# Optimization experiments

Hardware: AMD Instinct MI355X
Metric: run time of the kernel (lower is better)

## Reference

```python
import jax, jax.numpy as jnp
import numpy as np

TOPK = 16  # module init arg
EPS = 1e-12  # F.normalize eps


def setup_inputs() -> dict:
    key = jax.random.key(0)
    k1, k2, k3 = jax.random.split(key, 3)
    b, c, h, w = 2, 256, 96, 96
    rc = max(c // 4, 16)  # reduced_channels = 64
    x = jax.random.normal(k1, (b, c, h, w), dtype=jnp.float32)
    # 1x1 convs are channel-mixing matmuls; store weights as [out_ch, in_ch]
    w_reduce = jax.random.normal(k2, (rc, c), dtype=jnp.float32) * 0.05
    w_proj = jax.random.normal(k3, (c, rc), dtype=jnp.float32) * 0.05
    return {"x": x, "w_reduce": w_reduce, "w_proj": w_proj}


def reference(x, w_reduce, w_proj):
    b, c, h, w = x.shape
    n = h * w
    # reduce: 1x1 conv == channel matmul -> [b, rc, N]
    feat = jnp.einsum('rc,bchw->brhw', w_reduce, x).reshape(b, -1, n)
    # F.normalize(dim=1): divide by max(L2-norm over channels, eps)
    nrm = jnp.maximum(jnp.sqrt(jnp.sum(feat * feat, axis=1, keepdims=True)), EPS)
    nf = jnp.transpose(feat / nrm, (0, 2, 1))  # [b, N, rc]
    # cosine similarity matrix [b, N, N]
    sim = jnp.einsum('bnr,bmr->bnm', nf, nf)
    k = min(TOPK, n)
    _, idx = jax.lax.top_k(sim, k)  # [b, N, k]
    # gather top-k neighbor features and average -> [b, N, rc]
    corr = jax.vmap(lambda f, i: f[i].mean(axis=1))(nf, idx)
    # proj: 1x1 conv back to C channels, NCHW layout
    enhanced = jnp.einsum('cr,bnr->bnc', w_proj, corr)
    enhanced = jnp.transpose(enhanced, (0, 2, 1)).reshape(b, c, h, w)
    return x + enhanced
```

## Files before the change

kernel.cpp:

```cpp
#include <hip/hip_runtime.h>
#include <cstdint>
#include <cstddef>

#define NPIX 9216
#define NB 2
#define NC 256
#define RC 64
#define TK 16
#define NROWS (NB * NPIX)
#define CT 128
#define ECOLS 1152
#define NTE 9
#define MAXC 128
#define MARGIN 0.008f

typedef unsigned short ushort_t;
typedef unsigned int uint_t;
typedef __bf16 bf16x8 __attribute__((ext_vector_type(8)));
typedef float f32x4 __attribute__((ext_vector_type(4)));

__device__ __forceinline__ uint_t f2bf(float x) {
  uint_t u = __float_as_uint(x);
  return (u + 0x7FFFu + ((u >> 16) & 1u)) >> 16;
}

__device__ __forceinline__ uint_t ordu(float v) {
  uint_t u = __float_as_uint(v);
  return (u & 0x80000000u) ? ~u : (u | 0x80000000u);
}

__global__ __launch_bounds__(256) void k_reduce(
    const float* __restrict__ x, const float* __restrict__ wr,
    float* __restrict__ feat4) {
  __shared__ float wl[64 * 16];
  const int bi = blockIdx.x;
  const int pg = bi >> 4, rq = (bi >> 2) & 3, cq = bi & 3;
  const int tid = threadIdx.x;
  {
    const int cl = tid >> 2, rg = (tid & 3) * 4;
#pragma unroll
    for (int i = 0; i < 4; ++i)
      wl[cl * 16 + rg + i] = wr[(size_t)(rq * 16 + rg + i) * NC + cq * 64 + cl];
  }
  __syncthreads();

  const int p = pg * 256 + tid;
  const int b = p >= NPIX;
  const int n = p - b * NPIX;
  const float* xp = x + (size_t)b * NC * NPIX + (size_t)cq * 64 * NPIX + n;

  float4 acc[4];
#pragma unroll
  for (int i = 0; i < 4; ++i) acc[i] = make_float4(0.f, 0.f, 0.f, 0.f);

  for (int c = 0; c < 64; ++c) {
    const float xv = xp[(size_t)c * NPIX];
    const float4* w4 = (const float4*)(wl + c * 16);
#pragma unroll
    for (int i = 0; i < 4; ++i) {
      float4 w = w4[i];
      acc[i].x += w.x * xv; acc[i].y += w.y * xv;
      acc[i].z += w.z * xv; acc[i].w += w.w * xv;
    }
  }
  float4* o = (float4*)(feat4 + (((size_t)(rq * 4 + cq)) * NROWS + p) * 16);
#pragma unroll
  for (int i = 0; i < 4; ++i) o[i] = acc[i];
}

__global__ __launch_bounds__(256) void k_normsplit(
    const float* __restrict__ feat4, float* __restrict__ nf,
    ushort_t* __restrict__ hi) {
  const int t = blockIdx.x * 256 + threadIdx.x;
  const int p = t >> 2, q = t & 3;
  float4 v[4];
#pragma unroll
  for (int i = 0; i < 4; ++i) v[i] = make_float4(0.f, 0.f, 0.f, 0.f);
#pragma unroll
  for (int pt = 0; pt < 4; ++pt) {
    const float4* fp = (const float4*)(feat4 + (((size_t)(q * 4 + pt)) * NROWS + p) * 16);
#pragma unroll
    for (int i = 0; i < 4; ++i) {
      float4 a = fp[i];
      v[i].x += a.x; v[i].y += a.y; v[i].z += a.z; v[i].w += a.w;
    }
  }
  float ssq = 0.f;
#pragma unroll
  for (int i = 0; i < 4; ++i)
    ssq += v[i].x * v[i].x + v[i].y * v[i].y + v[i].z * v[i].z + v[i].w * v[i].w;
  ssq += __shfl_xor(ssq, 1);
  ssq += __shfl_xor(ssq, 2);
  const float inv = 1.f / fmaxf(sqrtf(ssq), 1e-12f);

  float s[16];
#pragma unroll
  for (int i = 0; i < 4; ++i) {
    s[i * 4 + 0] = v[i].x * inv; s[i * 4 + 1] = v[i].y * inv;
    s[i * 4 + 2] = v[i].z * inv; s[i * 4 + 3] = v[i].w * inv;
  }
  float4* no = (float4*)(nf + (size_t)p * RC + q * 16);
#pragma unroll
  for (int i = 0; i < 4; ++i)
    no[i] = make_float4(s[i * 4], s[i * 4 + 1], s[i * 4 + 2], s[i * 4 + 3]);

  uint_t hs[16];
#pragma unroll
  for (int i = 0; i < 16; ++i) hs[i] = f2bf(s[i]);
  uint4* ho = (uint4*)(hi + (size_t)p * RC + q * 16);
#pragma unroll
  for (int h = 0; h < 2; ++h)
    ho[h] = make_uint4(hs[h*8+0] | (hs[h*8+1] << 16), hs[h*8+2] | (hs[h*8+3] << 16),
                       hs[h*8+4] | (hs[h*8+5] << 16), hs[h*8+6] | (hs[h*8+7] << 16));
}

__global__ __launch_bounds__(256) void k_sim_max(
    const ushort_t* __restrict__ nf_hi, float* __restrict__ tmax) {
  __shared__ ushort_t sh[CT * 72];
  const int rb = blockIdx.x >> 3, q = blockIdx.x & 7;
  const int tid = threadIdx.x, wave = tid >> 6, lane = tid & 63;
  const int n = lane & 15, quad = lane >> 4;
  const int r0 = rb * 128 + wave * 32 + n, r1 = r0 + 16;
  const int b = rb >= 72;
  const size_t cbase = (size_t)b * NPIX;

  const bf16x8 bh00 = *(const bf16x8*)(nf_hi + (size_t)r0 * 64 + quad * 8);
  const bf16x8 bh01 = *(const bf16x8*)(nf_hi + (size_t)r0 * 64 + 32 + quad * 8);
  const bf16x8 bh10 = *(const bf16x8*)(nf_hi + (size_t)r1 * 64 + quad * 8);
  const bf16x8 bh11 = *(const bf16x8*)(nf_hi + (size_t)r1 * 64 + 32 + quad * 8);

  const int sc = tid >> 1, sseg = (tid & 1) * 32;
  float cm0 = -1e30f, cm1 = -1e30f;

  for (int t = 0; t < NTE; ++t) {
    const int cb = q * ECOLS + t * CT;
    __syncthreads();
    {
      const uint4* g = (const uint4*)(nf_hi + (cbase + cb + sc) * 64 + sseg);
      uint4* d = (uint4*)(sh + sc * 72 + sseg);
#pragma unroll
      for (int i = 0; i < 4; ++i) d[i] = g[i];
    }
    __syncthreads();

#pragma unroll 2
    for (int st = 0; st < 8; ++st) {
      const ushort_t* ap = sh + (st * 16 + n) * 72 + quad * 8;
      bf16x8 ah0 = *(const bf16x8*)ap;
      bf16x8 ah1 = *(const bf16x8*)(ap + 32);
      f32x4 z = {0.f, 0.f, 0.f, 0.f};
      f32x4 a0 = __builtin_amdgcn_mfma_f32_16x16x32_bf16(ah0, bh00, z, 0, 0, 0);
      a0 = __builtin_amdgcn_mfma_f32_16x16x32_bf16(ah1, bh01, a0, 0, 0, 0);
      f32x4 a1 = __builtin_amdgcn_mfma_f32_16x16x32_bf16(ah0, bh10, z, 0, 0, 0);
      a1 = __builtin_amdgcn_mfma_f32_16x16x32_bf16(ah1, bh11, a1, 0, 0, 0);
      cm0 = fmaxf(cm0, fmaxf(fmaxf(a0[0], a0[1]), fmaxf(a0[2], a0[3])));
      cm1 = fmaxf(cm1, fmaxf(fmaxf(a1[0], a1[1]), fmaxf(a1[2], a1[3])));
    }
    if (t % 3 == 2) {
      const int cn = t / 3;
      tmax[(size_t)r0 * 96 + (q * 4 + quad) * 3 + cn] = cm0;
      tmax[(size_t)r1 * 96 + (q * 4 + quad) * 3 + cn] = cm1;
      cm0 = -1e30f; cm1 = -1e30f;
    }
  }
}

__global__ __launch_bounds__(256) void k_thresh(
    const float* __restrict__ tmax, float* __restrict__ Tb) {
  const int wave = threadIdx.x >> 6, lane = threadIdx.x & 63;
  const int row = blockIdx.x * 4 + wave;
  const float* tp = tmax + (size_t)row * 96;
  float v0 = tp[lane];
  float v1 = (lane < 32) ? tp[64 + lane] : -1e30f;
  float m = -1e30f;
#pragma unroll
  for (int k = 0; k < TK; ++k) {
    float c = fmaxf(v0, v1);
#pragma unroll
    for (int d = 1; d < 64; d <<= 1) c = fmaxf(c, __shfl_xor(c, d));
    m = c;
    if (v0 == m) v0 = -1e30f;
    if (v1 == m) v1 = -1e30f;
  }
  if (lane == 0) Tb[row] = m - MARGIN;
}

__global__ __launch_bounds__(256) void k_collect(
    const ushort_t* __restrict__ nf_hi, const float* __restrict__ Tb,
    int* __restrict__ cidx, int* __restrict__ rowcnt) {
  __shared__ ushort_t sh[CT * 72];
  const int rb = blockIdx.x >> 3, q = blockIdx.x & 7;
  const int tid = threadIdx.x, wave = tid >> 6, lane = tid & 63;
  const int n = lane & 15, quad = lane >> 4;
  const int r0 = rb * 128 + wave * 32 + n, r1 = r0 + 16;
  const int b = rb >= 72;
  const size_t cbase = (size_t)b * NPIX;

  const bf16x8 bh00 = *(const bf16x8*)(nf_hi + (size_t)r0 * 64 + quad * 8);
  const bf16x8 bh01 = *(const bf16x8*)(nf_hi + (size_t)r0 * 64 + 32 + quad * 8);
  const bf16x8 bh10 = *(const bf16x8*)(nf_hi + (size_t)r1 * 64 + quad * 8);
  const bf16x8 bh11 = *(const bf16x8*)(nf_hi + (size_t)r1 * 64 + 32 + quad * 8);

  const float T0 = Tb[r0], T1 = Tb[r1];
  const int sc = tid >> 1, sseg = (tid & 1) * 32;

  for (int t = 0; t < NTE; ++t) {
    const int cb = q * ECOLS + t * CT;
    __syncthreads();
    {
      const uint4* g = (const uint4*)(nf_hi + (cbase + cb + sc) * 64 + sseg);
      uint4* d = (uint4*)(sh + sc * 72 + sseg);
#pragma unroll
      for (int i = 0; i < 4; ++i) d[i] = g[i];
    }
    __syncthreads();

#pragma unroll 2
    for (int st = 0; st < 8; ++st) {
      const ushort_t* ap = sh + (st * 16 + n) * 72 + quad * 8;
      bf16x8 ah0 = *(const bf16x8*)ap;
      bf16x8 ah1 = *(const bf16x8*)(ap + 32);
      f32x4 z = {0.f, 0.f, 0.f, 0.f};
      f32x4 a0 = __builtin_amdgcn_mfma_f32_16x16x32_bf16(ah0, bh00, z, 0, 0, 0);
      a0 = __builtin_amdgcn_mfma_f32_16x16x32_bf16(ah1, bh01, a0, 0, 0, 0);
      f32x4 a1 = __builtin_amdgcn_mfma_f32_16x16x32_bf16(ah0, bh10, z, 0, 0, 0);
      a1 = __builtin_amdgcn_mfma_f32_16x16x32_bf16(ah1, bh11, a1, 0, 0, 0);

      const int c0 = cb + st * 16 + quad * 4;
      const float mx0 = fmaxf(fmaxf(a0[0], a0[1]), fmaxf(a0[2], a0[3]));
      if (mx0 >= T0) {
#pragma unroll
        for (int r = 0; r < 4; ++r)
          if (a0[r] >= T0) {
            const int slot = atomicAdd(rowcnt + r0, 1);
            if (slot < MAXC) cidx[(size_t)r0 * MAXC + slot] = c0 + r;
          }
      }
      const float mx1 = fmaxf(fmaxf(a1[0], a1[1]), fmaxf(a1[2], a1[3]));
      if (mx1 >= T1) {
#pragma unroll
        for (int r = 0; r < 4; ++r)
          if (a1[r] >= T1) {
            const int slot = atomicAdd(rowcnt + r1, 1);
            if (slot < MAXC) cidx[(size_t)r1 * MAXC + slot] = c0 + r;
          }
      }
    }
  }
}

__global__ __launch_bounds__(256) void k_merge_gather(
    const float* __restrict__ nf, const int* __restrict__ cidx,
    const int* __restrict__ rowcnt, float* __restrict__ corr) {
  const int wave = threadIdx.x >> 6, lane = threadIdx.x & 63;
  const int row0 = blockIdx.x * 16 + wave * 4;
#pragma unroll 1
  for (int rr = 0; rr < 4; ++rr) {
    const int row = row0 + rr;
    const int b = row >= NPIX;
    const int rl = row - b * NPIX;
    const float* nfb = nf + (size_t)b * NPIX * RC;
    const int C = min(rowcnt[row], MAXC);

    float4 rv[16];
    const float4* r4 = (const float4*)(nf + (size_t)row * RC);
#pragma unroll
    for (int i = 0; i < 16; ++i) rv[i] = r4[i];

    const int* cp = cidx + (size_t)row * MAXC;
    unsigned long long k0 = 0, k1 = 0;
    {
      const int c0 = (lane < C) ? cp[lane] : rl;
      const float4* g = (const float4*)(nfb + (size_t)c0 * RC);
      float s = 0.f;
#pragma unroll
      for (int i = 0; i < 16; ++i) {
        float4 a = g[i];
        s += a.x * rv[i].x + a.y * rv[i].y + a.z * rv[i].z + a.w * rv[i].w;
      }
      if (lane < C)
        k0 = ((unsigned long long)ordu(s) << 32) | (uint_t)(~(uint_t)c0);
    }
    if (C > 64) {
      const int c1 = (64 + lane < C) ? cp[64 + lane] : rl;
      const float4* g = (const float4*)(nfb + (size_t)c1 * RC);
      float s = 0.f;
#pragma unroll
      for (int i = 0; i < 16; ++i) {
        float4 a = g[i];
        s += a.x * rv[i].x + a.y * rv[i].y + a.z * rv[i].z + a.w * rv[i].w;
      }
      if (64 + lane < C)
        k1 = ((unsigned long long)ordu(s) << 32) | (uint_t)(~(uint_t)c1);
    }

    int sel[TK];
#pragma unroll
    for (int t = 0; t < TK; ++t) {
      unsigned long long m = k0 > k1 ? k0 : k1;
#pragma unroll
      for (int d = 1; d < 64; d <<= 1) {
        unsigned long long o = __shfl_xor(m, d);
        m = (o > m) ? o : m;
      }
      sel[t] = (m == 0) ? rl : (int)(~(uint_t)(m & 0xFFFFFFFFull));
      if (k0 == m) k0 = 0;
      else if (k1 == m) k1 = 0;
    }

    float acc = 0.f;
#pragma unroll
    for (int t = 0; t < TK; ++t)
      acc += nfb[(size_t)sel[t] * RC + lane];
    corr[(size_t)row * RC + lane] = acc * 0.0625f;
  }
}

__global__ __launch_bounds__(256) void k_proj_add(
    const float* __restrict__ x, const float* __restrict__ wp,
    const float* __restrict__ corr, float* __restrict__ out) {
  const int pg = blockIdx.x >> 3, cq = blockIdx.x & 7;
  const int tid = threadIdx.x;

  __shared__ float wl[32 * RC];
  {
    const float4* src = (const float4*)(wp + (size_t)cq * 32 * RC);
    float4* dst = (float4*)wl;
#pragma unroll
    for (int i = 0; i < 2; ++i) dst[i * 256 + tid] = src[i * 256 + tid];
  }

  const int p = pg * 256 + tid;
  const int b = p >= NPIX;
  const int n = p - b * NPIX;

  float4 cr[16];
  const float4* c4 = (const float4*)(corr + (size_t)p * RC);
#pragma unroll
  for (int i = 0; i < 16; ++i) cr[i] = c4[i];
  __syncthreads();

  const size_t xb = (size_t)b * NC * NPIX + n;
  for (int cl = 0; cl < 32; ++cl) {
    const float4* w4 = (const float4*)(wl + cl * RC);
    float s = 0.f;
#pragma unroll
    for (int i = 0; i < 16; ++i) {
      float4 w = w4[i];
      s += w.x * cr[i].x + w.y * cr[i].y + w.z * cr[i].z + w.w * cr[i].w;
    }
    const int c = cq * 32 + cl;
    const size_t oi = xb + (size_t)c * NPIX;
    out[oi] = x[oi] + s;
  }
}

extern "C" void kernel_launch(void* const* d_in, const int* in_sizes, int n_in,
                              void* d_out, int out_size, void* d_ws, size_t ws_size,
                              hipStream_t stream) {
  const float* x = (const float*)d_in[0];
  const float* wr = (const float*)d_in[1];
  const float* wp = (const float*)d_in[2];
  float* out = (float*)d_out;

  char* ws = (char*)d_ws;
  float* feat4 = (float*)ws;
  float* tmax = (float*)ws;
  float* corr = (float*)ws;
  float* nf = (float*)(ws + 18874368);
  ushort_t* nf_hi = (ushort_t*)(ws + 23592960);
  float* Tb = (float*)(ws + 25952256);
  int* rowcnt = (int*)(ws + 26025984);
  int* cidx = (int*)(ws + 26099712);

  hipLaunchKernelGGL(k_reduce, dim3(1152), dim3(256), 0, stream, x, wr, feat4);
  hipLaunchKernelGGL(k_normsplit, dim3(288), dim3(256), 0, stream, feat4, nf, nf_hi);
  hipLaunchKernelGGL(k_sim_max, dim3(1152), dim3(256), 0, stream, nf_hi, tmax);
  hipLaunchKernelGGL(k_thresh, dim3(NROWS / 4), dim3(256), 0, stream, tmax, Tb);
  hipMemsetAsync(rowcnt, 0, NROWS * sizeof(int), stream);
  hipLaunchKernelGGL(k_collect, dim3(1152), dim3(256), 0, stream,
                     nf_hi, Tb, cidx, rowcnt);
  hipLaunchKernelGGL(k_merge_gather, dim3(1152), dim3(256), 0, stream,
                     nf, cidx, rowcnt, corr);
  hipLaunchKernelGGL(k_proj_add, dim3(576), dim3(256), 0, stream, x, wp, corr, out);
}
```

Baseline: 314.9 us.

## Restructure sim tiles: waves split columns, all rows in registers, swizzled LDS

In the similarity-max and collect kernels, each wave now holds B fragments for all 128 rows of the block and covers two 16-column strips of the staged tile. Before, each wave held 32 rows and swept all 128 columns. Shared memory drops its 72-element padding in favour of an XOR swizzle to avoid bank conflicts. Collect now issues one atomic per 4-value group using popcount instead of one per hit. Merge-gather maps one row per wave across more blocks. The chunk-max layout grows from 96 to 128 chunks per row, which changes the threshold input, and the larger register footprint may lower occupancy.

```diff
diff --git a/kernel.cpp b/kernel.cpp
--- a/kernel.cpp
+++ b/kernel.cpp
@@ -9,8 +9,10 @@
 #define TK 16
 #define NROWS (NB * NPIX)
 #define CT 128
+#define NQ 8
 #define ECOLS 1152
 #define NTE 9
+#define NCHUNK 128
 #define MAXC 128
 #define MARGIN 0.008f
 
@@ -114,64 +116,77 @@
                        hs[h*8+4] | (hs[h*8+5] << 16), hs[h*8+6] | (hs[h*8+7] << 16));
 }
 
+__device__ __forceinline__ void stage_tile(
+    const ushort_t* __restrict__ nf_hi, size_t cbase, int cb,
+    ushort_t* sh, int tid) {
+  const int srow = tid >> 1, shalf = tid & 1;
+  const uint4* g4 = (const uint4*)(nf_hi + (cbase + (size_t)(cb + srow)) * 64 + shalf * 32);
+  uint4 v0 = g4[0], v1 = g4[1], v2 = g4[2], v3 = g4[3];
+  ushort_t* rowp = sh + srow * 64;
+  const int rx = srow & 7;
+  *(uint4*)(rowp + (((shalf * 4 + 0) ^ rx) * 8)) = v0;
+  *(uint4*)(rowp + (((shalf * 4 + 1) ^ rx) * 8)) = v1;
+  *(uint4*)(rowp + (((shalf * 4 + 2) ^ rx) * 8)) = v2;
+  *(uint4*)(rowp + (((shalf * 4 + 3) ^ rx) * 8)) = v3;
+}
+
 __global__ __launch_bounds__(256) void k_sim_max(
     const ushort_t* __restrict__ nf_hi, float* __restrict__ tmax) {
-  __shared__ ushort_t sh[CT * 72];
+  __shared__ ushort_t sh[CT * 64];
   const int rb = blockIdx.x >> 3, q = blockIdx.x & 7;
   const int tid = threadIdx.x, wave = tid >> 6, lane = tid & 63;
   const int n = lane & 15, quad = lane >> 4;
-  const int r0 = rb * 128 + wave * 32 + n, r1 = r0 + 16;
+  const int rowbase = rb * 128 + n;
   const int b = rb >= 72;
   const size_t cbase = (size_t)b * NPIX;
 
-  const bf16x8 bh00 = *(const bf16x8*)(nf_hi + (size_t)r0 * 64 + quad * 8);
-  const bf16x8 bh01 = *(const bf16x8*)(nf_hi + (size_t)r0 * 64 + 32 + quad * 8);
-  const bf16x8 bh10 = *(const bf16x8*)(nf_hi + (size_t)r1 * 64 + quad * 8);
-  const bf16x8 bh11 = *(const bf16x8*)(nf_hi + (size_t)r1 * 64 + 32 + quad * 8);
-
-  const int sc = tid >> 1, sseg = (tid & 1) * 32;
-  float cm0 = -1e30f, cm1 = -1e30f;
+  bf16x8 bh0[8], bh1[8];
+#pragma unroll
+  for (int g = 0; g < 8; ++g) {
+    const ushort_t* rp = nf_hi + (size_t)(rowbase + g * 16) * 64;
+    bh0[g] = *(const bf16x8*)(rp + quad * 8);
+    bh1[g] = *(const bf16x8*)(rp + 32 + quad * 8);
+  }
+
+  const int x0 = (quad ^ (n & 7)) * 8;
+  const int x1 = ((quad + 4) ^ (n & 7)) * 8;
+
+  float cm[8];
+#pragma unroll
+  for (int g = 0; g < 8; ++g) cm[g] = -1e30f;
 
   for (int t = 0; t < NTE; ++t) {
-    const int cb = q * ECOLS + t * CT;
     __syncthreads();
-    {
-      const uint4* g = (const uint4*)(nf_hi + (cbase + cb + sc) * 64 + sseg);
-      uint4* d = (uint4*)(sh + sc * 72 + sseg);
-#pragma unroll
-      for (int i = 0; i < 4; ++i) d[i] = g[i];
-    }
+    stage_tile(nf_hi, cbase, q * ECOLS + t * CT, sh, tid);
     __syncthreads();
 
-#pragma unroll 2
-    for (int st = 0; st < 8; ++st) {
-      const ushort_t* ap = sh + (st * 16 + n) * 72 + quad * 8;
-      bf16x8 ah0 = *(const bf16x8*)ap;
-      bf16x8 ah1 = *(const bf16x8*)(ap + 32);
-      f32x4 z = {0.f, 0.f, 0.f, 0.f};
-      f32x4 a0 = __builtin_amdgcn_mfma_f32_16x16x32_bf16(ah0, bh00, z, 0, 0, 0);
-      a0 = __builtin_amdgcn_mfma_f32_16x16x32_bf16(ah1, bh01, a0, 0, 0, 0);
-      f32x4 a1 = __builtin_amdgcn_mfma_f32_16x16x32_bf16(ah0, bh10, z, 0, 0, 0);
-      a1 = __builtin_amdgcn_mfma_f32_16x16x32_bf16(ah1, bh11, a1, 0, 0, 0);
-      cm0 = fmaxf(cm0, fmaxf(fmaxf(a0[0], a0[1]), fmaxf(a0[2], a0[3])));
-      cm1 = fmaxf(cm1, fmaxf(fmaxf(a1[0], a1[1]), fmaxf(a1[2], a1[3])));
-    }
-    if (t % 3 == 2) {
-      const int cn = t / 3;
-      tmax[(size_t)r0 * 96 + (q * 4 + quad) * 3 + cn] = cm0;
-      tmax[(size_t)r1 * 96 + (q * 4 + quad) * 3 + cn] = cm1;
-      cm0 = -1e30f; cm1 = -1e30f;
-    }
-  }
+#pragma unroll
+    for (int p = 0; p < 2; ++p) {
+      const int st = wave * 2 + p;
+      const ushort_t* ap = sh + (st * 16 + n) * 64;
+      const bf16x8 ah0 = *(const bf16x8*)(ap + x0);
+      const bf16x8 ah1 = *(const bf16x8*)(ap + x1);
+#pragma unroll
+      for (int g = 0; g < 8; ++g) {
+        f32x4 z = {0.f, 0.f, 0.f, 0.f};
+        f32x4 a = __builtin_amdgcn_mfma_f32_16x16x32_bf16(ah0, bh0[g], z, 0, 0, 0);
+        a = __builtin_amdgcn_mfma_f32_16x16x32_bf16(ah1, bh1[g], a, 0, 0, 0);
+        cm[g] = fmaxf(fmaxf(a[0], a[1]), fmaxf(fmaxf(a[2], a[3]), cm[g]));
+      }
+    }
+  }
+#pragma unroll
+  for (int g = 0; g < 8; ++g)
+    tmax[(size_t)(rowbase + g * 16) * NCHUNK + q * 16 + wave * 4 + quad] = cm[g];
 }
 
 __global__ __launch_bounds__(256) void k_thresh(
     const float* __restrict__ tmax, float* __restrict__ Tb) {
   const int wave = threadIdx.x >> 6, lane = threadIdx.x & 63;
   const int row = blockIdx.x * 4 + wave;
-  const float* tp = tmax + (size_t)row * 96;
+  const float* tp = tmax + (size_t)row * NCHUNK;
   float v0 = tp[lane];
-  float v1 = (lane < 32) ? tp[64 + lane] : -1e30f;
+  float v1 = tp[64 + lane];
   float m = -1e30f;
 #pragma unroll
   for (int k = 0; k < TK; ++k) {
@@ -188,62 +203,58 @@
 __global__ __launch_bounds__(256) void k_collect(
     const ushort_t* __restrict__ nf_hi, const float* __restrict__ Tb,
     int* __restrict__ cidx, int* __restrict__ rowcnt) {
-  __shared__ ushort_t sh[CT * 72];
+  __shared__ ushort_t sh[CT * 64];
   const int rb = blockIdx.x >> 3, q = blockIdx.x & 7;
   const int tid = threadIdx.x, wave = tid >> 6, lane = tid & 63;
   const int n = lane & 15, quad = lane >> 4;
-  const int r0 = rb * 128 + wave * 32 + n, r1 = r0 + 16;
+  const int rowbase = rb * 128 + n;
   const int b = rb >= 72;
   const size_t cbase = (size_t)b * NPIX;
 
-  const bf16x8 bh00 = *(const bf16x8*)(nf_hi + (size_t)r0 * 64 + quad * 8);
-  const bf16x8 bh01 = *(const bf16x8*)(nf_hi + (size_t)r0 * 64 + 32 + quad * 8);
-  const bf16x8 bh10 = *(const bf16x8*)(nf_hi + (size_t)r1 * 64 + quad * 8);
-  const bf16x8 bh11 = *(const bf16x8*)(nf_hi + (size_t)r1 * 64 + 32 + quad * 8);
-
-  const float T0 = Tb[r0], T1 = Tb[r1];
-  const int sc = tid >> 1, sseg = (tid & 1) * 32;
+  bf16x8 bh0[8], bh1[8];
+  float T[8];
+#pragma unroll
+  for (int g = 0; g < 8; ++g) {
+    const ushort_t* rp = nf_hi + (size_t)(rowbase + g * 16) * 64;
+    bh0[g] = *(const bf16x8*)(rp + quad * 8);
+    bh1[g] = *(const bf16x8*)(rp + 32 + quad * 8);
+    T[g] = Tb[rowbase + g * 16];
+  }
+
+  const int x0 = (quad ^ (n & 7)) * 8;
+  const int x1 = ((quad + 4) ^ (n & 7)) * 8;
 
   for (int t = 0; t < NTE; ++t) {
     const int cb = q * ECOLS + t * CT;
     __syncthreads();
-    {
-      const uint4* g = (const uint4*)(nf_hi + (cbase + cb + sc) * 64 + sseg);
-      uint4* d = (uint4*)(sh + sc * 72 + sseg);
-#pragma unroll
-      for (int i = 0; i < 4; ++i) d[i] = g[i];
-    }
+    stage_tile(nf_hi, cbase, cb, sh, tid);
     __syncthreads();
 
-#pragma unroll 2
-    for (int st = 0; st < 8; ++st) {
-      const ushort_t* ap = sh + (st * 16 + n) * 72 + quad * 8;
-      bf16x8 ah0 = *(const bf16x8*)ap;
-      bf16x8 ah1 = *(const bf16x8*)(ap + 32);
-      f32x4 z = {0.f, 0.f, 0.f, 0.f};
-      f32x4 a0 = __builtin_amdgcn_mfma_f32_16x16x32_bf16(ah0, bh00, z, 0, 0, 0);
-      a0 = __builtin_amdgcn_mfma_f32_16x16x32_bf16(ah1, bh01, a0, 0, 0, 0);
-      f32x4 a1 = __builtin_amdgcn_mfma_f32_16x16x32_bf16(ah0, bh10, z, 0, 0, 0);
-      a1 = __builtin_amdgcn_mfma_f32_16x16x32_bf16(ah1, bh11, a1, 0, 0, 0);
-
+#pragma unroll
+    for (int p = 0; p < 2; ++p) {
+      const int st = wave * 2 + p;
+      const ushort_t* ap = sh + (st * 16 + n) * 64;
+      const bf16x8 ah0 = *(const bf16x8*)(ap + x0);
+      const bf16x8 ah1 = *(const bf16x8*)(ap + x1);
       const int c0 = cb + st * 16 + quad * 4;
-      const float mx0 = fmaxf(fmaxf(a0[0], a0[1]), fmaxf(a0[2], a0[3]));
-      if (mx0 >= T0) {
-#pragma unroll
-        for (int r = 0; r < 4; ++r)
-          if (a0[r] >= T0) {
-            const int slot = atomicAdd(rowcnt + r0, 1);
-            if (slot < MAXC) cidx[(size_t)r0 * MAXC + slot] = c0 + r;
-          }
-      }
-      const float mx1 = fmaxf(fmaxf(a1[0], a1[1]), fmaxf(a1[2], a1[3]));
-      if (mx1 >= T1) {
-#pragma unroll
-        for (int r = 0; r < 4; ++r)
-          if (a1[r] >= T1) {
-            const int slot = atomicAdd(rowcnt + r1, 1);
-            if (slot < MAXC) cidx[(size_t)r1 * MAXC + slot] = c0 + r;
-          }
+#pragma unroll
+      for (int g = 0; g < 8; ++g) {
+        f32x4 z = {0.f, 0.f, 0.f, 0.f};
+        f32x4 a = __builtin_amdgcn_mfma_f32_16x16x32_bf16(ah0, bh0[g], z, 0, 0, 0);
+        a = __builtin_amdgcn_mfma_f32_16x16x32_bf16(ah1, bh1[g], a, 0, 0, 0);
+        const float Tg = T[g];
+        const int m = (a[0] >= Tg) | ((a[1] >= Tg) << 1) |
+                      ((a[2] >= Tg) << 2) | ((a[3] >= Tg) << 3);
+        if (m) {
+          const int rg = rowbase + g * 16;
+          int slot = atomicAdd(rowcnt + rg, __popc(m));
+#pragma unroll
+          for (int r = 0; r < 4; ++r)
+            if (m & (1 << r)) {
+              if (slot < MAXC) cidx[(size_t)rg * MAXC + slot] = c0 + r;
+              ++slot;
+            }
+        }
       }
     }
   }
@@ -253,67 +264,63 @@
     const float* __restrict__ nf, const int* __restrict__ cidx,
     const int* __restrict__ rowcnt, float* __restrict__ corr) {
   const int wave = threadIdx.x >> 6, lane = threadIdx.x & 63;
-  const int row0 = blockIdx.x * 16 + wave * 4;
-#pragma unroll 1
-  for (int rr = 0; rr < 4; ++rr) {
-    const int row = row0 + rr;
-    const int b = row >= NPIX;
-    const int rl = row - b * NPIX;
-    const float* nfb = nf + (size_t)b * NPIX * RC;
-    const int C = min(rowcnt[row], MAXC);
-
-    float4 rv[16];
-    const float4* r4 = (const float4*)(nf + (size_t)row * RC);
-#pragma unroll
-    for (int i = 0; i < 16; ++i) rv[i] = r4[i];
-
-    const int* cp = cidx + (size_t)row * MAXC;
-    unsigned long long k0 = 0, k1 = 0;
-    {
-      const int c0 = (lane < C) ? cp[lane] : rl;
-      const float4* g = (const float4*)(nfb + (size_t)c0 * RC);
-      float s = 0.f;
-#pragma unroll
-      for (int i = 0; i < 16; ++i) {
-        float4 a = g[i];
-        s += a.x * rv[i].x + a.y * rv[i].y + a.z * rv[i].z + a.w * rv[i].w;
-      }
-      if (lane < C)
-        k0 = ((unsigned long long)ordu(s) << 32) | (uint_t)(~(uint_t)c0);
-    }
-    if (C > 64) {
-      const int c1 = (64 + lane < C) ? cp[64 + lane] : rl;
-      const float4* g = (const float4*)(nfb + (size_t)c1 * RC);
-      float s = 0.f;
-#pragma unroll
-      for (int i = 0; i < 16; ++i) {
-        float4 a = g[i];
-        s += a.x * rv[i].x + a.y * rv[i].y + a.z * rv[i].z + a.w * rv[i].w;
-      }
-      if (64 + lane < C)
-        k1 = ((unsigned long long)ordu(s) << 32) | (uint_t)(~(uint_t)c1);
-    }
-
-    int sel[TK];
-#pragma unroll
-    for (int t = 0; t < TK; ++t) {
-      unsigned long long m = k0 > k1 ? k0 : k1;
-#pragma unroll
-      for (int d = 1; d < 64; d <<= 1) {
-        unsigned long long o = __shfl_xor(m, d);
-        m = (o > m) ? o : m;
-      }
-      sel[t] = (m == 0) ? rl : (int)(~(uint_t)(m & 0xFFFFFFFFull));
-      if (k0 == m) k0 = 0;
-      else if (k1 == m) k1 = 0;
-    }
-
-    float acc = 0.f;
-#pragma unroll
-    for (int t = 0; t < TK; ++t)
-      acc += nfb[(size_t)sel[t] * RC + lane];
-    corr[(size_t)row * RC + lane] = acc * 0.0625f;
-  }
+  const int row = blockIdx.x * 4 + wave;
+  const int b = row >= NPIX;
+  const int rl = row - b * NPIX;
+  const float* nfb = nf + (size_t)b * NPIX * RC;
+  const int C = min(rowcnt[row], MAXC);
+
+  float4 rv[16];
+  const float4* r4 = (const float4*)(nf + (size_t)row * RC);
+#pragma unroll
+  for (int i = 0; i < 16; ++i) rv[i] = r4[i];
+
+  const int* cp = cidx + (size_t)row * MAXC;
+  unsigned long long k0 = 0, k1 = 0;
+  {
+    const int c0 = (lane < C) ? cp[lane] : rl;
+    const float4* g = (const float4*)(nfb + (size_t)c0 * RC);
+    float s = 0.f;
+#pragma unroll
+    for (int i = 0; i < 16; ++i) {
+      float4 a = g[i];
+      s += a.x * rv[i].x + a.y * rv[i].y + a.z * rv[i].z + a.w * rv[i].w;
+    }
+    if (lane < C)
+      k0 = ((unsigned long long)ordu(s) << 32) | (uint_t)(~(uint_t)c0);
+  }
+  if (C > 64) {
+    const int c1 = (64 + lane < C) ? cp[64 + lane] : rl;
+    const float4* g = (const float4*)(nfb + (size_t)c1 * RC);
+    float s = 0.f;
+#pragma unroll
+    for (int i = 0; i < 16; ++i) {
+      float4 a = g[i];
+      s += a.x * rv[i].x + a.y * rv[i].y + a.z * rv[i].z + a.w * rv[i].w;
+    }
+    if (64 + lane < C)
+      k1 = ((unsigned long long)ordu(s) << 32) | (uint_t)(~(uint_t)c1);
+  }
+
+  int sel[TK];
+#pragma unroll
+  for (int t = 0; t < TK; ++t) {
+    unsigned long long m = k0 > k1 ? k0 : k1;
+#pragma unroll
+    for (int d = 1; d < 64; d <<= 1) {
+      unsigned long long o = __shfl_xor(m, d);
+      m = (o > m) ? o : m;
+    }
+    sel[t] = (m == 0) ? rl : (int)(~(uint_t)(m & 0xFFFFFFFFull));
+    if (k0 == m) k0 = 0;
+    else if (k1 == m) k1 = 0;
+  }
+
+  float acc = 0.f;
+#pragma unroll
+  for (int t = 0; t < TK; ++t)
+    acc += nfb[(size_t)sel[t] * RC + lane];
+  corr[(size_t)row * RC + lane] = acc * 0.0625f;
 }
 
 __global__ __launch_bounds__(256) void k_proj_add(
@@ -380,7 +387,7 @@
   hipMemsetAsync(rowcnt, 0, NROWS * sizeof(int), stream);
   hipLaunchKernelGGL(k_collect, dim3(1152), dim3(256), 0, stream,
                      nf_hi, Tb, cidx, rowcnt);
-  hipLaunchKernelGGL(k_merge_gather, dim3(1152), dim3(256), 0, stream,
+  hipLaunchKernelGGL(k_merge_gather, dim3(NROWS / 4), dim3(256), 0, stream,
                      nf, cidx, rowcnt, corr);
   hipLaunchKernelGGL(k_proj_add, dim3(576), dim3(256), 0, stream, x, wp, corr, out);
 }
```

Result: slower. 366.3 us (+16.3%).

## Buffer candidates in LDS and replace iterative top-k with radix-select ballot

Applied to the files above, without the earlier changes.

k_collect now appends candidate columns to per-row shared-memory lists using one LDS atomic per group of hits. Each row block then flushes its lists to global memory with a single global atomic per row, replacing one global atomic per hit. k_merge_gather assigns one row per wave and selects the 16 largest keys with a 64-bit bitwise radix search built on ballots, instead of 16 rounds of shuffle-based max reduction. This adds LDS use and a 64-step ballot loop. Ties at the threshold could produce a different ordering of selected indices, but the mean over the selected rows does not depend on order.

```diff
diff --git a/kernel.cpp b/kernel.cpp
--- a/kernel.cpp
+++ b/kernel.cpp
@@ -12,6 +12,7 @@
 #define ECOLS 1152
 #define NTE 9
 #define MAXC 128
+#define LCAP 128
 #define MARGIN 0.008f
 
 typedef unsigned short ushort_t;
@@ -189,12 +190,17 @@
     const ushort_t* __restrict__ nf_hi, const float* __restrict__ Tb,
     int* __restrict__ cidx, int* __restrict__ rowcnt) {
   __shared__ ushort_t sh[CT * 72];
+  __shared__ ushort_t lst[128][LCAP + 1];
+  __shared__ int lcnt[128];
   const int rb = blockIdx.x >> 3, q = blockIdx.x & 7;
   const int tid = threadIdx.x, wave = tid >> 6, lane = tid & 63;
   const int n = lane & 15, quad = lane >> 4;
-  const int r0 = rb * 128 + wave * 32 + n, r1 = r0 + 16;
+  const int rl0 = wave * 32 + n, rl1 = rl0 + 16;
+  const int r0 = rb * 128 + rl0, r1 = r0 + 16;
   const int b = rb >= 72;
   const size_t cbase = (size_t)b * NPIX;
+
+  if (tid < 128) lcnt[tid] = 0;
 
   const bf16x8 bh00 = *(const bf16x8*)(nf_hi + (size_t)r0 * 64 + quad * 8);
   const bf16x8 bh01 = *(const bf16x8*)(nf_hi + (size_t)r0 * 64 + 32 + quad * 8);
@@ -227,24 +233,38 @@
       a1 = __builtin_amdgcn_mfma_f32_16x16x32_bf16(ah1, bh11, a1, 0, 0, 0);
 
       const int c0 = cb + st * 16 + quad * 4;
-      const float mx0 = fmaxf(fmaxf(a0[0], a0[1]), fmaxf(a0[2], a0[3]));
-      if (mx0 >= T0) {
+      const int m0 = (a0[0] >= T0) | ((a0[1] >= T0) << 1) |
+                     ((a0[2] >= T0) << 2) | ((a0[3] >= T0) << 3);
+      if (m0) {
+        int slot = atomicAdd(&lcnt[rl0], __popc(m0));
 #pragma unroll
         for (int r = 0; r < 4; ++r)
-          if (a0[r] >= T0) {
-            const int slot = atomicAdd(rowcnt + r0, 1);
-            if (slot < MAXC) cidx[(size_t)r0 * MAXC + slot] = c0 + r;
+          if (m0 & (1 << r)) {
+            if (slot < LCAP) lst[rl0][slot] = (ushort_t)(c0 + r);
+            ++slot;
           }
       }
-      const float mx1 = fmaxf(fmaxf(a1[0], a1[1]), fmaxf(a1[2], a1[3]));
-      if (mx1 >= T1) {
+      const int m1 = (a1[0] >= T1) | ((a1[1] >= T1) << 1) |
+                     ((a1[2] >= T1) << 2) | ((a1[3] >= T1) << 3);
+      if (m1) {
+        int slot = atomicAdd(&lcnt[rl1], __popc(m1));
 #pragma unroll
         for (int r = 0; r < 4; ++r)
-          if (a1[r] >= T1) {
-            const int slot = atomicAdd(rowcnt + r1, 1);
-            if (slot < MAXC) cidx[(size_t)r1 * MAXC + slot] = c0 + r;
+          if (m1 & (1 << r)) {
+            if (slot < LCAP) lst[rl1][slot] = (ushort_t)(c0 + r);
+            ++slot;
           }
       }
+    }
+  }
+  __syncthreads();
+  if (tid < 128) {
+    const int row = rb * 128 + tid;
+    const int cnt = min(lcnt[tid], LCAP);
+    int base = atomicAdd(rowcnt + row, cnt);
+    for (int j = 0; j < cnt; ++j) {
+      const int gs = base + j;
+      if (gs < MAXC) cidx[(size_t)row * MAXC + gs] = (int)lst[tid][j];
     }
   }
 }
@@ -252,68 +272,78 @@
 __global__ __launch_bounds__(256) void k_merge_gather(
     const float* __restrict__ nf, const int* __restrict__ cidx,
     const int* __restrict__ rowcnt, float* __restrict__ corr) {
+  __shared__ ushort_t selc[4][TK];
   const int wave = threadIdx.x >> 6, lane = threadIdx.x & 63;
-  const int row0 = blockIdx.x * 16 + wave * 4;
-#pragma unroll 1
-  for (int rr = 0; rr < 4; ++rr) {
-    const int row = row0 + rr;
-    const int b = row >= NPIX;
-    const int rl = row - b * NPIX;
-    const float* nfb = nf + (size_t)b * NPIX * RC;
-    const int C = min(rowcnt[row], MAXC);
-
-    float4 rv[16];
-    const float4* r4 = (const float4*)(nf + (size_t)row * RC);
-#pragma unroll
-    for (int i = 0; i < 16; ++i) rv[i] = r4[i];
-
-    const int* cp = cidx + (size_t)row * MAXC;
-    unsigned long long k0 = 0, k1 = 0;
-    {
-      const int c0 = (lane < C) ? cp[lane] : rl;
-      const float4* g = (const float4*)(nfb + (size_t)c0 * RC);
-      float s = 0.f;
-#pragma unroll
-      for (int i = 0; i < 16; ++i) {
-        float4 a = g[i];
-        s += a.x * rv[i].x + a.y * rv[i].y + a.z * rv[i].z + a.w * rv[i].w;
-      }
-      if (lane < C)
-        k0 = ((unsigned long long)ordu(s) << 32) | (uint_t)(~(uint_t)c0);
-    }
-    if (C > 64) {
-      const int c1 = (64 + lane < C) ? cp[64 + lane] : rl;
-      const float4* g = (const float4*)(nfb + (size_t)c1 * RC);
-      float s = 0.f;
-#pragma unroll
-      for (int i = 0; i < 16; ++i) {
-        float4 a = g[i];
-        s += a.x * rv[i].x + a.y * rv[i].y + a.z * rv[i].z + a.w * rv[i].w;
-      }
-      if (64 + lane < C)
-        k1 = ((unsigned long long)ordu(s) << 32) | (uint_t)(~(uint_t)c1);
-    }
-
-    int sel[TK];
-#pragma unroll
-    for (int t = 0; t < TK; ++t) {
-      unsigned long long m = k0 > k1 ? k0 : k1;
-#pragma unroll
-      for (int d = 1; d < 64; d <<= 1) {
-        unsigned long long o = __shfl_xor(m, d);
-        m = (o > m) ? o : m;
-      }
-      sel[t] = (m == 0) ? rl : (int)(~(uint_t)(m & 0xFFFFFFFFull));
-      if (k0 == m) k0 = 0;
-      else if (k1 == m) k1 = 0;
-    }
-
-    float acc = 0.f;
-#pragma unroll
-    for (int t = 0; t < TK; ++t)
-      acc += nfb[(size_t)sel[t] * RC + lane];
-    corr[(size_t)row * RC + lane] = acc * 0.0625f;
-  }
+  const int row = blockIdx.x * 4 + wave;
+  const int b = row >= NPIX;
+  const int rl = row - b * NPIX;
+  const float* nfb = nf + (size_t)b * NPIX * RC;
+  const int C = min(rowcnt[row], MAXC);
+
+  if (lane < TK) selc[wave][lane] = (ushort_t)rl;
+  __syncthreads();
+
+  float4 rv[16];
+  const float4* r4 = (const float4*)(nf + (size_t)row * RC);
+#pragma unroll
+  for (int i = 0; i < 16; ++i) rv[i] = r4[i];
+
+  const int* cp = cidx + (size_t)row * MAXC;
+  unsigned long long k0 = 0, k1 = 0;
+  int c0 = rl, c1 = rl;
+  {
+    c0 = (lane < C) ? cp[lane] : rl;
+    const float4* g = (const float4*)(nfb + (size_t)c0 * RC);
+    float s = 0.f;
+#pragma unroll
+    for (int i = 0; i < 16; ++i) {
+      float4 a = g[i];
+      s += a.x * rv[i].x + a.y * rv[i].y + a.z * rv[i].z + a.w * rv[i].w;
+    }
+    if (lane < C)
+      k0 = ((unsigned long long)ordu(s) << 32) | (uint_t)(~(uint_t)c0);
+  }
+  if (C > 64) {
+    c1 = (64 + lane < C) ? cp[64 + lane] : rl;
+    const float4* g = (const float4*)(nfb + (size_t)c1 * RC);
+    float s = 0.f;
+#pragma unroll
+    for (int i = 0; i < 16; ++i) {
+      float4 a = g[i];
+      s += a.x * rv[i].x + a.y * rv[i].y + a.z * rv[i].z + a.w * rv[i].w;
+    }
+    if (64 + lane < C)
+      k1 = ((unsigned long long)ordu(s) << 32) | (uint_t)(~(uint_t)c1);
+  }
+
+  unsigned long long thr = 0;
+#pragma unroll
+  for (int bit = 63; bit >= 0; --bit) {
+    const unsigned long long cand = thr | (1ull << bit);
+    const int cnt = __popcll(__ballot(k0 >= cand)) + __popcll(__ballot(k1 >= cand));
+    if (cnt >= TK) thr = cand;
+  }
+  if (thr != 0) {
+    const unsigned long long ml = (lane == 0) ? 0ull : (~0ull >> (64 - lane));
+    const unsigned long long b0 = __ballot(k0 >= thr);
+    const unsigned long long b1 = __ballot(k1 >= thr);
+    const int n0 = __popcll(b0);
+    if (k0 >= thr) {
+      const int r = __popcll(b0 & ml);
+      if (r < TK) selc[wave][r] = (ushort_t)c0;
+    }
+    if (k1 >= thr) {
+      const int r = n0 + __popcll(b1 & ml);
+      if (r < TK) selc[wave][r] = (ushort_t)c1;
+    }
+  }
+  __syncthreads();
+
+  float acc = 0.f;
+#pragma unroll
+  for (int t = 0; t < TK; ++t)
+    acc += nfb[(size_t)selc[wave][t] * RC + lane];
+  corr[(size_t)row * RC + lane] = acc * 0.0625f;
 }
 
 __global__ __launch_bounds__(256) void k_proj_add(
@@ -380,7 +410,7 @@
   hipMemsetAsync(rowcnt, 0, NROWS * sizeof(int), stream);
   hipLaunchKernelGGL(k_collect, dim3(1152), dim3(256), 0, stream,
                      nf_hi, Tb, cidx, rowcnt);
-  hipLaunchKernelGGL(k_merge_gather, dim3(1152), dim3(256), 0, stream,
+  hipLaunchKernelGGL(k_merge_gather, dim3(NROWS / 4), dim3(256), 0, stream,
                      nf, cidx, rowcnt, corr);
   hipLaunchKernelGGL(k_proj_add, dim3(576), dim3(256), 0, stream, x, wp, corr, out);
 }
```

Measured after the change: 279.6 us. 1.13x faster.
